# Kernel optimization log

Hardware: AMD Instinct MI355X
Metric: run time of the kernel (lower is better)

The kernel has to match this reference:

```python
import jax, jax.numpy as jnp
import numpy as np

D = 1024
H = 16
HD = D // H
MLP = 4 * D
EPS = 1e-5


def layer_norm(x, g, b):
    mu = jnp.mean(x, axis=-1, keepdims=True)
    var = jnp.mean((x - mu) ** 2, axis=-1, keepdims=True)
    return (x - mu) * jax.lax.rsqrt(var + EPS) * g + b


def grn(stacked, W, b, g, be):
    # stacked: [B, L, S, D]; input-dependent weights + normalized branch, summed over L
    w = jax.nn.relu(jnp.einsum('blsd,de->blse', stacked, W) + b)
    n = layer_norm(stacked, g, be)
    return jnp.sum(w + n, axis=1)  # [B, S, D]


def setup_inputs() -> dict:
    key = jax.random.key(0)
    ks = jax.random.split(key, 24)
    s = 0.02
    inp = {
        'x': jax.random.normal(ks[0], (2, 2048, D), jnp.float32),
        'layer_outputs': jax.random.normal(ks[1], (2, 4, 2048, D), jnp.float32),
    }
    i = 2
    for name in ('q', 'k', 'v'):
        inp[f'grn_{name}_W'] = jax.random.normal(ks[i], (D, D), jnp.float32) * s; i += 1
        inp[f'grn_{name}_b'] = jnp.zeros((D,), jnp.float32)
        inp[f'grn_{name}_g'] = jnp.ones((D,), jnp.float32)
        inp[f'grn_{name}_be'] = jnp.zeros((D,), jnp.float32)
    inp['attn_out_W'] = jax.random.normal(ks[i], (D, D), jnp.float32) * s; i += 1
    inp['attn_out_b'] = jnp.zeros((D,), jnp.float32)
    inp['attn_norm_g'] = jnp.ones((D,), jnp.float32)
    inp['attn_norm_b'] = jnp.zeros((D,), jnp.float32)
    inp['ffn_W1'] = jax.random.normal(ks[i], (D, MLP), jnp.float32) * s; i += 1
    inp['ffn_b1'] = jnp.zeros((MLP,), jnp.float32)
    inp['ffn_W2'] = jax.random.normal(ks[i], (MLP, D), jnp.float32) * s; i += 1
    inp['ffn_b2'] = jnp.zeros((D,), jnp.float32)
    inp['ffn_norm_g'] = jnp.ones((D,), jnp.float32)
    inp['ffn_norm_b'] = jnp.zeros((D,), jnp.float32)
    return inp


def reference(x, layer_outputs,
              grn_q_W, grn_q_b, grn_q_g, grn_q_be,
              grn_k_W, grn_k_b, grn_k_g, grn_k_be,
              grn_v_W, grn_v_b, grn_v_g, grn_v_be,
              attn_out_W, attn_out_b, attn_norm_g, attn_norm_b,
              ffn_W1, ffn_b1, ffn_W2, ffn_b2, ffn_norm_g, ffn_norm_b):
    B, S, _ = x.shape
    q = grn(layer_outputs, grn_q_W, grn_q_b, grn_q_g, grn_q_be)
    k = grn(layer_outputs, grn_k_W, grn_k_b, grn_k_g, grn_k_be)
    v = grn(layer_outputs, grn_v_W, grn_v_b, grn_v_g, grn_v_be)
    # [B, H, S, HD]
    q = q.reshape(B, S, H, HD).transpose(0, 2, 1, 3)
    k = k.reshape(B, S, H, HD).transpose(0, 2, 1, 3)
    v = v.reshape(B, S, H, HD).transpose(0, 2, 1, 3)
    scale = HD ** -0.5
    attn = jnp.einsum('bhqd,bhkd->bhqk', q, k) * scale
    attn = jax.nn.softmax(attn, axis=-1)
    out = jnp.einsum('bhqk,bhkd->bhqd', attn, v)
    out = out.transpose(0, 2, 1, 3).reshape(B, S, D)
    out = out @ attn_out_W + attn_out_b
    out = x + layer_norm(out, attn_norm_g, attn_norm_b)
    h = jax.nn.gelu(out @ ffn_W1 + ffn_b1, approximate=False) @ ffn_W2 + ffn_b2
    out = out + layer_norm(h, ffn_norm_g, ffn_norm_b)
    return out
```

## Files before the change

### kernel.cpp

```cpp
#include <hip/hip_runtime.h>
#include <cstddef>

#define B_  2
#define S_  2048
#define D_  1024
#define L_  4
#define H_  16
#define HD_ 64
#define MLP_ 4096
#define EPS_ 1e-5f

typedef __attribute__((ext_vector_type(8))) short  bf16x8;
typedef __attribute__((ext_vector_type(4))) float  f32x4;

__device__ __forceinline__ unsigned short f2bf(float x) {
    unsigned int u = __float_as_uint(x);
    u = (u + 0x7fffu + ((u >> 16) & 1u)) >> 16;
    return (unsigned short)u;
}
__device__ __forceinline__ float bf2f(unsigned short h) {
    return __uint_as_float(((unsigned int)h) << 16);
}

__global__ __launch_bounds__(256) void wconv_kernel(
    const float* __restrict__ W, unsigned short* __restrict__ Thi,
    unsigned short* __restrict__ Tlo, int K, int N)
{
    __shared__ float T[32][33];
    const int n0 = blockIdx.x * 32, k0 = blockIdx.y * 32;
    const int t = threadIdx.x;
    {
        const int r = t >> 3, c4 = (t & 7) * 4;
        const float4 w = *(const float4*)(W + (size_t)(k0 + r) * N + n0 + c4);
        T[r][c4 + 0] = w.x; T[r][c4 + 1] = w.y;
        T[r][c4 + 2] = w.z; T[r][c4 + 3] = w.w;
    }
    __syncthreads();
    {
        const int n = t >> 3, k4 = (t & 7) * 4;
        ushort4 h, l;
        float f;
        f = T[k4 + 0][n]; h.x = f2bf(f); l.x = f2bf(f - bf2f(h.x));
        f = T[k4 + 1][n]; h.y = f2bf(f); l.y = f2bf(f - bf2f(h.y));
        f = T[k4 + 2][n]; h.z = f2bf(f); l.z = f2bf(f - bf2f(h.z));
        f = T[k4 + 3][n]; h.w = f2bf(f); l.w = f2bf(f - bf2f(h.w));
        *(ushort4*)(Thi + (size_t)(n0 + n) * K + k0 + k4) = h;
        *(ushort4*)(Tlo + (size_t)(n0 + n) * K + k0 + k4) = l;
    }
}

template <int EPI>
__global__ __launch_bounds__(256) void gemm_bf16s_kernel(
    const float* __restrict__ A,
    const unsigned short* __restrict__ Bth, const unsigned short* __restrict__ Btl,
    const float* __restrict__ bias, float* __restrict__ C,
    int M, int N, int K)
{
    __shared__ unsigned short As_hi[128 * 40];
    __shared__ unsigned short As_lo[128 * 40];
    __shared__ unsigned short Bs_hi[128 * 40];
    __shared__ unsigned short Bs_lo[128 * 40];

    const int tid  = threadIdx.x;
    const int lane = tid & 63;
    const int wid  = tid >> 6;
    const int wr   = wid >> 1, wc = wid & 1;
    const int l15  = lane & 15, chunk = lane >> 4;
    const int row0 = blockIdx.y * 128;
    const int col0 = blockIdx.x * 128;

    const int a_off = (wr * 64 + l15) * 40 + chunk * 8;
    const int b_off = (wc * 64 + l15) * 40 + chunk * 8;

    f32x4 acc[4][4] = {};

    for (int k0 = 0; k0 < K; k0 += 32) {
        __syncthreads();
        #pragma unroll
        for (int u = 0; u < 4; ++u) {
            const int idx = tid + u * 256;
            const int r  = idx >> 3;
            const int kc = (idx & 7) * 4;
            const float4 a = *(const float4*)(A + (size_t)(row0 + r) * K + k0 + kc);
            ushort4 h, l;
            h.x = f2bf(a.x); l.x = f2bf(a.x - bf2f(h.x));
            h.y = f2bf(a.y); l.y = f2bf(a.y - bf2f(h.y));
            h.z = f2bf(a.z); l.z = f2bf(a.z - bf2f(h.z));
            h.w = f2bf(a.w); l.w = f2bf(a.w - bf2f(h.w));
            *(ushort4*)&As_hi[r * 40 + kc] = h;
            *(ushort4*)&As_lo[r * 40 + kc] = l;
        }
        #pragma unroll
        for (int u = 0; u < 2; ++u) {
            const int idx = tid + u * 256;
            const int c  = idx >> 2;
            const int kc = (idx & 3) * 8;
            const size_t gb = (size_t)(col0 + c) * K + k0 + kc;
            *(uint4*)&Bs_hi[c * 40 + kc] = *(const uint4*)(Bth + gb);
            *(uint4*)&Bs_lo[c * 40 + kc] = *(const uint4*)(Btl + gb);
        }
        __syncthreads();

        bf16x8 ah[4], al[4], bh[4], bl[4];
        #pragma unroll
        for (int mi = 0; mi < 4; ++mi) {
            ah[mi] = *(const bf16x8*)&As_hi[a_off + mi * 640];
            al[mi] = *(const bf16x8*)&As_lo[a_off + mi * 640];
        }
        #pragma unroll
        for (int ni = 0; ni < 4; ++ni) {
            bh[ni] = *(const bf16x8*)&Bs_hi[b_off + ni * 640];
            bl[ni] = *(const bf16x8*)&Bs_lo[b_off + ni * 640];
        }
        #pragma unroll
        for (int mi = 0; mi < 4; ++mi)
            #pragma unroll
            for (int ni = 0; ni < 4; ++ni) {
                acc[mi][ni] = __builtin_amdgcn_mfma_f32_16x16x32_bf16(
                    ah[mi], bh[ni], acc[mi][ni], 0, 0, 0);
                acc[mi][ni] = __builtin_amdgcn_mfma_f32_16x16x32_bf16(
                    ah[mi], bl[ni], acc[mi][ni], 0, 0, 0);
                acc[mi][ni] = __builtin_amdgcn_mfma_f32_16x16x32_bf16(
                    al[mi], bh[ni], acc[mi][ni], 0, 0, 0);
            }
    }

    const int rbase = row0 + wr * 64 + (lane >> 4) * 4;
    const int cbase = col0 + wc * 64 + l15;
    #pragma unroll
    for (int mi = 0; mi < 4; ++mi) {
        #pragma unroll
        for (int reg = 0; reg < 4; ++reg) {
            const int gr = rbase + mi * 16 + reg;
            #pragma unroll
            for (int ni = 0; ni < 4; ++ni) {
                const int gc = cbase + ni * 16;
                float v = acc[mi][ni][reg] + bias[gc];
                if (EPI == 1) v = fmaxf(v, 0.f);
                else if (EPI == 2) v = 0.5f * v * (1.f + erff(v * 0.70710678118654752f));
                C[(size_t)gr * N + gc] = v;
            }
        }
    }
}

__global__ __launch_bounds__(256) void grn_ns_kernel(
    const float* __restrict__ LO, float* __restrict__ NS)
{
    const int row = blockIdx.x;
    const int b = row >> 11, s = row & (S_ - 1);
    const int tid = threadIdx.x;
    __shared__ float r1[4], r2[4];

    float acc[4] = {0.f, 0.f, 0.f, 0.f};
    #pragma unroll
    for (int l = 0; l < L_; ++l) {
        const float* xr = LO + ((size_t)((b * L_ + l) * S_ + s)) * D_;
        const float4 v = *(const float4*)(xr + tid * 4);
        float s1 = v.x + v.y + v.z + v.w;
        float s2 = v.x * v.x + v.y * v.y + v.z * v.z + v.w * v.w;
        #pragma unroll
        for (int off = 32; off >= 1; off >>= 1) {
            s1 += __shfl_xor(s1, off);
            s2 += __shfl_xor(s2, off);
        }
        if ((tid & 63) == 0) { r1[tid >> 6] = s1; r2[tid >> 6] = s2; }
        __syncthreads();
        s1 = r1[0] + r1[1] + r1[2] + r1[3];
        s2 = r2[0] + r2[1] + r2[2] + r2[3];
        __syncthreads();
        const float mu  = s1 * (1.f / D_);
        const float var = s2 * (1.f / D_) - mu * mu;
        const float rs  = rsqrtf(var + EPS_);
        acc[0] += (v.x - mu) * rs;
        acc[1] += (v.y - mu) * rs;
        acc[2] += (v.z - mu) * rs;
        acc[3] += (v.w - mu) * rs;
    }
    float4 o = {acc[0], acc[1], acc[2], acc[3]};
    *(float4*)(NS + (size_t)row * D_ + tid * 4) = o;
}

__global__ __launch_bounds__(256) void grn_reduce_kernel(
    const float* __restrict__ P, const float* __restrict__ NS,
    const float* __restrict__ g, const float* __restrict__ be,
    float* __restrict__ out)
{
    const size_t i4 = (size_t)blockIdx.x * 256 + threadIdx.x;
    const int d4 = (int)(i4 & (D_ / 4 - 1));
    const size_t row = i4 >> 8;
    const int b = (int)(row >> 11), s = (int)(row & (S_ - 1));

    float4 a = {0.f, 0.f, 0.f, 0.f};
    #pragma unroll
    for (int l = 0; l < L_; ++l) {
        const float4 w = *(const float4*)(P + ((size_t)((b * L_ + l) * S_ + s)) * D_ + d4 * 4);
        a.x += w.x; a.y += w.y; a.z += w.z; a.w += w.w;
    }
    const float4 n  = *(const float4*)(NS + row * D_ + d4 * 4);
    const float4 gg = *(const float4*)(g + d4 * 4);
    const float4 bb = *(const float4*)(be + d4 * 4);
    float4 o;
    o.x = a.x + n.x * gg.x + 4.f * bb.x;
    o.y = a.y + n.y * gg.y + 4.f * bb.y;
    o.z = a.z + n.z * gg.z + 4.f * bb.z;
    o.w = a.w + n.w * gg.w + 4.f * bb.w;
    *(float4*)(out + row * D_ + d4 * 4) = o;
}

__global__ __launch_bounds__(256) void kvconv_kernel(
    const float* __restrict__ Kin, const float* __restrict__ Vin,
    unsigned short* __restrict__ Kh, unsigned short* __restrict__ Kl,
    unsigned short* __restrict__ Vth, unsigned short* __restrict__ Vtl)
{
    __shared__ float T[64][68];
    const int t = threadIdx.x;
    const int st = blockIdx.x;
    const int bh = blockIdx.y;
    const int b = bh >> 4, h = bh & 15;
    const int s0 = st * 64;

    #pragma unroll
    for (int u = 0; u < 4; ++u) {
        const int idx = t + u * 256;
        const int r  = idx >> 4;
        const int c4 = (idx & 15) * 4;
        const size_t src = ((size_t)(b * S_ + s0 + r)) * D_ + h * 64 + c4;
        const float4 kf = *(const float4*)(Kin + src);
        ushort4 hh, ll;
        hh.x = f2bf(kf.x); ll.x = f2bf(kf.x - bf2f(hh.x));
        hh.y = f2bf(kf.y); ll.y = f2bf(kf.y - bf2f(hh.y));
        hh.z = f2bf(kf.z); ll.z = f2bf(kf.z - bf2f(hh.z));
        hh.w = f2bf(kf.w); ll.w = f2bf(kf.w - bf2f(hh.w));
        const size_t kd = ((size_t)bh * S_ + s0 + r) * 64 + c4;
        *(ushort4*)(Kh + kd) = hh;
        *(ushort4*)(Kl + kd) = ll;
        const float4 vf = *(const float4*)(Vin + src);
        T[r][c4 + 0] = vf.x; T[r][c4 + 1] = vf.y;
        T[r][c4 + 2] = vf.z; T[r][c4 + 3] = vf.w;
    }
    __syncthreads();
    #pragma unroll
    for (int u = 0; u < 4; ++u) {
        const int idx = t + u * 256;
        const int d  = idx >> 4;
        const int s4 = (idx & 15) * 4;
        ushort4 hh, ll;
        float f;
        f = T[s4 + 0][d]; hh.x = f2bf(f); ll.x = f2bf(f - bf2f(hh.x));
        f = T[s4 + 1][d]; hh.y = f2bf(f); ll.y = f2bf(f - bf2f(hh.y));
        f = T[s4 + 2][d]; hh.z = f2bf(f); ll.z = f2bf(f - bf2f(hh.z));
        f = T[s4 + 3][d]; hh.w = f2bf(f); ll.w = f2bf(f - bf2f(hh.w));
        const size_t vd = ((size_t)bh * 64 + d) * S_ + s0 + s4;
        *(ushort4*)(Vth + vd) = hh;
        *(ushort4*)(Vtl + vd) = ll;
    }
}

__global__ __launch_bounds__(256) void attn_mfma_kernel(
    const float* __restrict__ Q,
    const unsigned short* __restrict__ Kh, const unsigned short* __restrict__ Kl,
    const unsigned short* __restrict__ Vth, const unsigned short* __restrict__ Vtl,
    float* __restrict__ O)
{
    __shared__ unsigned short Ksh[64 * 72], Ksl[64 * 72];
    __shared__ unsigned short Vsh[64 * 72], Vsl[64 * 72];
    __shared__ unsigned short Phs[4][32 * 72];
    __shared__ unsigned short Pls[4][32 * 72];

    const int tid  = threadIdx.x;
    const int lane = tid & 63;
    const int w    = tid >> 6;
    const int l15  = lane & 15, g = lane >> 4;
    const int bh   = blockIdx.y;
    const int b    = bh >> 4, h = bh & 15;
    const int q0   = blockIdx.x * 128 + w * 32;
    const float scale = 0.125f;

    bf16x8 qh[2][2], ql[2][2];
    #pragma unroll
    for (int mi = 0; mi < 2; ++mi)
        #pragma unroll
        for (int ks = 0; ks < 2; ++ks) {
            const float* qp = Q + ((size_t)(b * S_ + q0 + mi * 16 + l15)) * D_
                              + h * 64 + ks * 32 + g * 8;
            const float4 f0 = *(const float4*)qp;
            const float4 f1 = *(const float4*)(qp + 4);
            const float vs[8] = {f0.x * scale, f0.y * scale, f0.z * scale, f0.w * scale,
                                 f1.x * scale, f1.y * scale, f1.z * scale, f1.w * scale};
            #pragma unroll
            for (int j = 0; j < 8; ++j) {
                const unsigned short hv = f2bf(vs[j]);
                qh[mi][ks][j] = (short)hv;
                ql[mi][ks][j] = (short)f2bf(vs[j] - bf2f(hv));
            }
        }

    f32x4 o[2][4] = {};
    float mrun[2][4], lrun[2][4];
    #pragma unroll
    for (int mi = 0; mi < 2; ++mi)
        #pragma unroll
        for (int r = 0; r < 4; ++r) { mrun[mi][r] = -1e30f; lrun[mi][r] = 0.f; }

    const unsigned short* KhB = Kh  + (size_t)bh * S_ * 64;
    const unsigned short* KlB = Kl  + (size_t)bh * S_ * 64;
    const unsigned short* VhB = Vth + (size_t)bh * 64 * S_;
    const unsigned short* VlB = Vtl + (size_t)bh * 64 * S_;

    for (int kt = 0; kt < S_; kt += 64) {
        __syncthreads();
        #pragma unroll
        for (int u = 0; u < 2; ++u) {
            const int idx = tid + u * 256;
            const int rr  = idx >> 3;
            const int c8  = (idx & 7) * 8;
            *(uint4*)&Ksh[rr * 72 + c8] = *(const uint4*)(KhB + (size_t)(kt + rr) * 64 + c8);
            *(uint4*)&Ksl[rr * 72 + c8] = *(const uint4*)(KlB + (size_t)(kt + rr) * 64 + c8);
            *(uint4*)&Vsh[rr * 72 + c8] = *(const uint4*)(VhB + (size_t)rr * S_ + kt + c8);
            *(uint4*)&Vsl[rr * 72 + c8] = *(const uint4*)(VlB + (size_t)rr * S_ + kt + c8);
        }
        __syncthreads();

        f32x4 s[2][4] = {};
        #pragma unroll
        for (int ks = 0; ks < 2; ++ks)
            #pragma unroll
            for (int ni = 0; ni < 4; ++ni) {
                const bf16x8 khf = *(const bf16x8*)&Ksh[(ni * 16 + l15) * 72 + ks * 32 + g * 8];
                const bf16x8 klf = *(const bf16x8*)&Ksl[(ni * 16 + l15) * 72 + ks * 32 + g * 8];
                #pragma unroll
                for (int mi = 0; mi < 2; ++mi) {
                    s[mi][ni] = __builtin_amdgcn_mfma_f32_16x16x32_bf16(qh[mi][ks], khf, s[mi][ni], 0, 0, 0);
                    s[mi][ni] = __builtin_amdgcn_mfma_f32_16x16x32_bf16(qh[mi][ks], klf, s[mi][ni], 0, 0, 0);
                    s[mi][ni] = __builtin_amdgcn_mfma_f32_16x16x32_bf16(ql[mi][ks], khf, s[mi][ni], 0, 0, 0);
                }
            }

        #pragma unroll
        for (int mi = 0; mi < 2; ++mi) {
            #pragma unroll
            for (int r = 0; r < 4; ++r) {
                float mx = fmaxf(fmaxf(s[mi][0][r], s[mi][1][r]),
                                 fmaxf(s[mi][2][r], s[mi][3][r]));
                mx = fmaxf(mx, __shfl_xor(mx, 1));
                mx = fmaxf(mx, __shfl_xor(mx, 2));
                mx = fmaxf(mx, __shfl_xor(mx, 4));
                mx = fmaxf(mx, __shfl_xor(mx, 8));
                const float mn = fmaxf(mrun[mi][r], mx);
                const float c  = __expf(mrun[mi][r] - mn);
                mrun[mi][r] = mn;
                float rs = 0.f;
                #pragma unroll
                for (int ni = 0; ni < 4; ++ni) {
                    const float p = __expf(s[mi][ni][r] - mn);
                    rs += p;
                    const unsigned short ph = f2bf(p);
                    const int off = (mi * 16 + 4 * g + r) * 72 + ni * 16 + l15;
                    Phs[w][off] = ph;
                    Pls[w][off] = f2bf(p - bf2f(ph));
                }
                rs += __shfl_xor(rs, 1);
                rs += __shfl_xor(rs, 2);
                rs += __shfl_xor(rs, 4);
                rs += __shfl_xor(rs, 8);
                lrun[mi][r] = lrun[mi][r] * c + rs;
                #pragma unroll
                for (int di = 0; di < 4; ++di) o[mi][di][r] *= c;
            }
        }

        #pragma unroll
        for (int ks = 0; ks < 2; ++ks) {
            bf16x8 pfh[2], pfl[2];
            #pragma unroll
            for (int mi = 0; mi < 2; ++mi) {
                pfh[mi] = *(const bf16x8*)&Phs[w][(mi * 16 + l15) * 72 + ks * 32 + g * 8];
                pfl[mi] = *(const bf16x8*)&Pls[w][(mi * 16 + l15) * 72 + ks * 32 + g * 8];
            }
            #pragma unroll
            for (int di = 0; di < 4; ++di) {
                const bf16x8 vhf = *(const bf16x8*)&Vsh[(di * 16 + l15) * 72 + ks * 32 + g * 8];
                const bf16x8 vlf = *(const bf16x8*)&Vsl[(di * 16 + l15) * 72 + ks * 32 + g * 8];
                #pragma unroll
                for (int mi = 0; mi < 2; ++mi) {
                    o[mi][di] = __builtin_amdgcn_mfma_f32_16x16x32_bf16(pfh[mi], vhf, o[mi][di], 0, 0, 0);
                    o[mi][di] = __builtin_amdgcn_mfma_f32_16x16x32_bf16(pfh[mi], vlf, o[mi][di], 0, 0, 0);
                    o[mi][di] = __builtin_amdgcn_mfma_f32_16x16x32_bf16(pfl[mi], vhf, o[mi][di], 0, 0, 0);
                }
            }
        }
    }

    #pragma unroll
    for (int mi = 0; mi < 2; ++mi)
        #pragma unroll
        for (int r = 0; r < 4; ++r) {
            const float inv = 1.f / lrun[mi][r];
            float* op = O + ((size_t)(b * S_ + q0 + mi * 16 + 4 * g + r)) * D_
                        + h * 64 + l15;
            #pragma unroll
            for (int di = 0; di < 4; ++di) op[di * 16] = o[mi][di][r] * inv;
        }
}

__global__ __launch_bounds__(256) void add_ln_kernel(
    const float* __restrict__ Y, const float* __restrict__ R,
    const float* __restrict__ g, const float* __restrict__ beta,
    float* __restrict__ out)
{
    const int row = blockIdx.x;
    const int tid = threadIdx.x;
    __shared__ float r1[4], r2[4];

    const float4 v = *(const float4*)(Y + (size_t)row * D_ + tid * 4);
    float s1 = v.x + v.y + v.z + v.w;
    float s2 = v.x * v.x + v.y * v.y + v.z * v.z + v.w * v.w;
    #pragma unroll
    for (int off = 32; off >= 1; off >>= 1) {
        s1 += __shfl_xor(s1, off);
        s2 += __shfl_xor(s2, off);
    }
    if ((tid & 63) == 0) { r1[tid >> 6] = s1; r2[tid >> 6] = s2; }
    __syncthreads();
    s1 = r1[0] + r1[1] + r1[2] + r1[3];
    s2 = r2[0] + r2[1] + r2[2] + r2[3];
    const float mu  = s1 * (1.f / D_);
    const float var = s2 * (1.f / D_) - mu * mu;
    const float rs  = rsqrtf(var + EPS_);

    const float4 rr = *(const float4*)(R + (size_t)row * D_ + tid * 4);
    const float4 gg = *(const float4*)(g + tid * 4);
    const float4 bb = *(const float4*)(beta + tid * 4);
    float4 o;
    o.x = rr.x + (v.x - mu) * rs * gg.x + bb.x;
    o.y = rr.y + (v.y - mu) * rs * gg.y + bb.y;
    o.z = rr.z + (v.z - mu) * rs * gg.z + bb.z;
    o.w = rr.w + (v.w - mu) * rs * gg.w + bb.w;
    *(float4*)(out + (size_t)row * D_ + tid * 4) = o;
}

extern "C" void kernel_launch(void* const* d_in, const int* in_sizes, int n_in,
                              void* d_out, int out_size, void* d_ws, size_t ws_size,
                              hipStream_t stream)
{
    const float* x  = (const float*)d_in[0];
    const float* LO = (const float*)d_in[1];
    const float* Wq  = (const float*)d_in[2];
    const float* bq_ = (const float*)d_in[3];
    const float* gq  = (const float*)d_in[4];
    const float* beq = (const float*)d_in[5];
    const float* Wk  = (const float*)d_in[6];
    const float* bk_ = (const float*)d_in[7];
    const float* gk  = (const float*)d_in[8];
    const float* bek = (const float*)d_in[9];
    const float* Wv  = (const float*)d_in[10];
    const float* bv_ = (const float*)d_in[11];
    const float* gv  = (const float*)d_in[12];
    const float* bev = (const float*)d_in[13];
    const float* Wo  = (const float*)d_in[14];
    const float* bo  = (const float*)d_in[15];
    const float* ang = (const float*)d_in[16];
    const float* anb = (const float*)d_in[17];
    const float* W1  = (const float*)d_in[18];
    const float* b1  = (const float*)d_in[19];
    const float* W2  = (const float*)d_in[20];
    const float* b2  = (const float*)d_in[21];
    const float* fng = (const float*)d_in[22];
    const float* fnb = (const float*)d_in[23];

    const size_t BS  = (size_t)B_ * S_;
    const size_t SEG = BS * D_;
    float* ws  = (float*)d_ws;
    float* ns   = ws;
    float* bufq = ws + SEG;
    float* bufk = ws + 2 * SEG;
    float* bufv = ws + 3 * SEG;
    float* big  = ws + 4 * SEG;

    unsigned short* wt = (unsigned short*)(ws + 8 * SEG);
    const size_t MM = 1048576;
    unsigned short* wtq_h = wt;            unsigned short* wtq_l = wt + MM;
    unsigned short* wtk_h = wt + 2 * MM;   unsigned short* wtk_l = wt + 3 * MM;
    unsigned short* wtv_h = wt + 4 * MM;   unsigned short* wtv_l = wt + 5 * MM;
    unsigned short* wto_h = wt + 6 * MM;   unsigned short* wto_l = wt + 7 * MM;
    unsigned short* w1_h  = wt + 8 * MM;   unsigned short* w1_l  = wt + 12 * MM;
    unsigned short* w2_h  = wt + 16 * MM;  unsigned short* w2_l  = wt + 20 * MM;

    const size_t KVSEG = (size_t)B_ * H_ * S_ * HD_;
    unsigned short* kv  = (unsigned short*)big;
    unsigned short* kh_ = kv;
    unsigned short* kl_ = kv + KVSEG;
    unsigned short* vth = kv + 2 * KVSEG;
    unsigned short* vtl = kv + 3 * KVSEG;

    const dim3 blk(256);

    wconv_kernel<<<dim3(32, 32),  blk, 0, stream>>>(Wq, wtq_h, wtq_l, D_, D_);
    wconv_kernel<<<dim3(32, 32),  blk, 0, stream>>>(Wk, wtk_h, wtk_l, D_, D_);
    wconv_kernel<<<dim3(32, 32),  blk, 0, stream>>>(Wv, wtv_h, wtv_l, D_, D_);
    wconv_kernel<<<dim3(32, 32),  blk, 0, stream>>>(Wo, wto_h, wto_l, D_, D_);
    wconv_kernel<<<dim3(128, 32), blk, 0, stream>>>(W1, w1_h,  w1_l,  D_, MLP_);
    wconv_kernel<<<dim3(32, 128), blk, 0, stream>>>(W2, w2_h,  w2_l,  MLP_, D_);

    grn_ns_kernel<<<dim3(BS), blk, 0, stream>>>(LO, ns);

    const unsigned short* Wh[3] = {wtq_h, wtk_h, wtv_h};
    const unsigned short* Wl[3] = {wtq_l, wtk_l, wtv_l};
    const float* bp[3]  = {bq_, bk_, bv_};
    const float* gp[3]  = {gq, gk, gv};
    const float* bep[3] = {beq, bek, bev};
    float* outp[3] = {bufq, bufk, bufv};
    for (int p = 0; p < 3; ++p) {
        gemm_bf16s_kernel<1><<<dim3(D_ / 128, (B_ * L_ * S_) / 128), blk, 0, stream>>>(
            LO, Wh[p], Wl[p], bp[p], big, B_ * L_ * S_, D_, D_);
        grn_reduce_kernel<<<dim3(BS), blk, 0, stream>>>(big, ns, gp[p], bep[p], outp[p]);
    }

    kvconv_kernel<<<dim3(S_ / 64, B_ * H_), blk, 0, stream>>>(bufk, bufv, kh_, kl_, vth, vtl);
    attn_mfma_kernel<<<dim3(S_ / 128, B_ * H_), blk, 0, stream>>>(bufq, kh_, kl_, vth, vtl, ns);

    gemm_bf16s_kernel<0><<<dim3(D_ / 128, BS / 128), blk, 0, stream>>>(
        ns, wto_h, wto_l, bo, bufq, (int)BS, D_, D_);

    add_ln_kernel<<<dim3(BS), blk, 0, stream>>>(bufq, x, ang, anb, bufk);

    gemm_bf16s_kernel<2><<<dim3(MLP_ / 128, BS / 128), blk, 0, stream>>>(
        bufk, w1_h, w1_l, b1, big, (int)BS, MLP_, D_);

    gemm_bf16s_kernel<0><<<dim3(D_ / 128, BS / 128), blk, 0, stream>>>(
        big, w2_h, w2_l, b2, bufv, (int)BS, D_, MLP_);

    add_ln_kernel<<<dim3(BS), blk, 0, stream>>>(bufv, bufk, fng, fnb, (float*)d_out);
}
```

Measured before the change: 1.223 ms.

## Pre-split GEMM activations to bf16 pairs, prefetch tiles, swizzle blocks, drop P low part

Activations are converted once to hi/lo bf16 pairs in a separate pass, or written that way by the FFN1 epilogue, so GEMMs load packed bf16 instead of converting fp32 per tile. The GEMM gains register prefetch of the next K tile, an XCD-aware block-index swizzle, and s_setprio around MFMA bursts. Attention drops the low-precision half of P, which removes one MFMA per PV step and its LDS buffer at some accuracy cost. The extra conversion passes add memory traffic and workspace use.

```diff
diff --git a/kernel.cpp b/kernel.cpp
--- a/kernel.cpp
+++ b/kernel.cpp
@@ -20,6 +20,21 @@
 }
 __device__ __forceinline__ float bf2f(unsigned short h) {
     return __uint_as_float(((unsigned int)h) << 16);
+}
+
+__global__ __launch_bounds__(256) void aconv_kernel(
+    const float* __restrict__ X, unsigned short* __restrict__ Xh,
+    unsigned short* __restrict__ Xl)
+{
+    const size_t i4 = (size_t)blockIdx.x * 256 + threadIdx.x;
+    const float4 v = *(const float4*)(X + i4 * 4);
+    ushort4 h, l;
+    h.x = f2bf(v.x); l.x = f2bf(v.x - bf2f(h.x));
+    h.y = f2bf(v.y); l.y = f2bf(v.y - bf2f(h.y));
+    h.z = f2bf(v.z); l.z = f2bf(v.z - bf2f(h.z));
+    h.w = f2bf(v.w); l.w = f2bf(v.w - bf2f(h.w));
+    *(ushort4*)(Xh + i4 * 4) = h;
+    *(ushort4*)(Xl + i4 * 4) = l;
 }
 
 __global__ __launch_bounds__(256) void wconv_kernel(
@@ -49,11 +64,12 @@
     }
 }
 
-template <int EPI>
-__global__ __launch_bounds__(256) void gemm_bf16s_kernel(
-    const float* __restrict__ A,
+template <int EPI, int OUT>
+__global__ __launch_bounds__(256) void gemm_bf16p_kernel(
+    const unsigned short* __restrict__ Ah, const unsigned short* __restrict__ Al,
     const unsigned short* __restrict__ Bth, const unsigned short* __restrict__ Btl,
     const float* __restrict__ bias, float* __restrict__ C,
+    unsigned short* __restrict__ Chi, unsigned short* __restrict__ Clo,
     int M, int N, int K)
 {
     __shared__ unsigned short As_hi[128 * 40];
@@ -66,40 +82,54 @@
     const int wid  = tid >> 6;
     const int wr   = wid >> 1, wc = wid & 1;
     const int l15  = lane & 15, chunk = lane >> 4;
-    const int row0 = blockIdx.y * 128;
-    const int col0 = blockIdx.x * 128;
+
+    const int NX   = N >> 7;
+    const int nblk = (M >> 7) * NX;
+    int bid = blockIdx.x;
+    if ((nblk & 7) == 0) bid = (bid & 7) * (nblk >> 3) + (bid >> 3);
+    const int row0 = (bid / NX) * 128;
+    const int col0 = (bid % NX) * 128;
 
     const int a_off = (wr * 64 + l15) * 40 + chunk * 8;
     const int b_off = (wc * 64 + l15) * 40 + chunk * 8;
 
+    const int sr  = tid >> 2;
+    const int skc = (tid & 3) * 8;
+
     f32x4 acc[4][4] = {};
+    uint4 ra_h[2], ra_l[2], rb_h[2], rb_l[2];
+
+    #pragma unroll
+    for (int u = 0; u < 2; ++u) {
+        const int r = sr + u * 64;
+        const size_t ga = (size_t)(row0 + r) * K + skc;
+        const size_t gb = (size_t)(col0 + r) * K + skc;
+        ra_h[u] = *(const uint4*)(Ah + ga);  ra_l[u] = *(const uint4*)(Al + ga);
+        rb_h[u] = *(const uint4*)(Bth + gb); rb_l[u] = *(const uint4*)(Btl + gb);
+    }
 
     for (int k0 = 0; k0 < K; k0 += 32) {
         __syncthreads();
         #pragma unroll
-        for (int u = 0; u < 4; ++u) {
-            const int idx = tid + u * 256;
-            const int r  = idx >> 3;
-            const int kc = (idx & 7) * 4;
-            const float4 a = *(const float4*)(A + (size_t)(row0 + r) * K + k0 + kc);
-            ushort4 h, l;
-            h.x = f2bf(a.x); l.x = f2bf(a.x - bf2f(h.x));
-            h.y = f2bf(a.y); l.y = f2bf(a.y - bf2f(h.y));
-            h.z = f2bf(a.z); l.z = f2bf(a.z - bf2f(h.z));
-            h.w = f2bf(a.w); l.w = f2bf(a.w - bf2f(h.w));
-            *(ushort4*)&As_hi[r * 40 + kc] = h;
-            *(ushort4*)&As_lo[r * 40 + kc] = l;
-        }
-        #pragma unroll
         for (int u = 0; u < 2; ++u) {
-            const int idx = tid + u * 256;
-            const int c  = idx >> 2;
-            const int kc = (idx & 3) * 8;
-            const size_t gb = (size_t)(col0 + c) * K + k0 + kc;
-            *(uint4*)&Bs_hi[c * 40 + kc] = *(const uint4*)(Bth + gb);
-            *(uint4*)&Bs_lo[c * 40 + kc] = *(const uint4*)(Btl + gb);
+            const int r = sr + u * 64;
+            *(uint4*)&As_hi[r * 40 + skc] = ra_h[u];
+            *(uint4*)&As_lo[r * 40 + skc] = ra_l[u];
+            *(uint4*)&Bs_hi[r * 40 + skc] = rb_h[u];
+            *(uint4*)&Bs_lo[r * 40 + skc] = rb_l[u];
         }
         __syncthreads();
+
+        if (k0 + 32 < K) {
+            #pragma unroll
+            for (int u = 0; u < 2; ++u) {
+                const int r = sr + u * 64;
+                const size_t ga = (size_t)(row0 + r) * K + k0 + 32 + skc;
+                const size_t gb = (size_t)(col0 + r) * K + k0 + 32 + skc;
+                ra_h[u] = *(const uint4*)(Ah + ga);  ra_l[u] = *(const uint4*)(Al + ga);
+                rb_h[u] = *(const uint4*)(Bth + gb); rb_l[u] = *(const uint4*)(Btl + gb);
+            }
+        }
 
         bf16x8 ah[4], al[4], bh[4], bl[4];
         #pragma unroll
@@ -112,6 +142,7 @@
             bh[ni] = *(const bf16x8*)&Bs_hi[b_off + ni * 640];
             bl[ni] = *(const bf16x8*)&Bs_lo[b_off + ni * 640];
         }
+        __builtin_amdgcn_s_setprio(1);
         #pragma unroll
         for (int mi = 0; mi < 4; ++mi)
             #pragma unroll
@@ -123,6 +154,7 @@
                 acc[mi][ni] = __builtin_amdgcn_mfma_f32_16x16x32_bf16(
                     al[mi], bh[ni], acc[mi][ni], 0, 0, 0);
             }
+        __builtin_amdgcn_s_setprio(0);
     }
 
     const int rbase = row0 + wr * 64 + (lane >> 4) * 4;
@@ -138,7 +170,13 @@
                 float v = acc[mi][ni][reg] + bias[gc];
                 if (EPI == 1) v = fmaxf(v, 0.f);
                 else if (EPI == 2) v = 0.5f * v * (1.f + erff(v * 0.70710678118654752f));
-                C[(size_t)gr * N + gc] = v;
+                if (OUT == 0) {
+                    C[(size_t)gr * N + gc] = v;
+                } else {
+                    const unsigned short hv = f2bf(v);
+                    Chi[(size_t)gr * N + gc] = hv;
+                    Clo[(size_t)gr * N + gc] = f2bf(v - bf2f(hv));
+                }
             }
         }
     }
@@ -266,7 +304,6 @@
     __shared__ unsigned short Ksh[64 * 72], Ksl[64 * 72];
     __shared__ unsigned short Vsh[64 * 72], Vsl[64 * 72];
     __shared__ unsigned short Phs[4][32 * 72];
-    __shared__ unsigned short Pls[4][32 * 72];
 
     const int tid  = threadIdx.x;
     const int lane = tid & 63;
@@ -329,12 +366,14 @@
             for (int ni = 0; ni < 4; ++ni) {
                 const bf16x8 khf = *(const bf16x8*)&Ksh[(ni * 16 + l15) * 72 + ks * 32 + g * 8];
                 const bf16x8 klf = *(const bf16x8*)&Ksl[(ni * 16 + l15) * 72 + ks * 32 + g * 8];
+                __builtin_amdgcn_s_setprio(1);
                 #pragma unroll
                 for (int mi = 0; mi < 2; ++mi) {
                     s[mi][ni] = __builtin_amdgcn_mfma_f32_16x16x32_bf16(qh[mi][ks], khf, s[mi][ni], 0, 0, 0);
                     s[mi][ni] = __builtin_amdgcn_mfma_f32_16x16x32_bf16(qh[mi][ks], klf, s[mi][ni], 0, 0, 0);
                     s[mi][ni] = __builtin_amdgcn_mfma_f32_16x16x32_bf16(ql[mi][ks], khf, s[mi][ni], 0, 0, 0);
                 }
+                __builtin_amdgcn_s_setprio(0);
             }
 
         #pragma unroll
@@ -355,10 +394,7 @@
                 for (int ni = 0; ni < 4; ++ni) {
                     const float p = __expf(s[mi][ni][r] - mn);
                     rs += p;
-                    const unsigned short ph = f2bf(p);
-                    const int off = (mi * 16 + 4 * g + r) * 72 + ni * 16 + l15;
-                    Phs[w][off] = ph;
-                    Pls[w][off] = f2bf(p - bf2f(ph));
+                    Phs[w][(mi * 16 + 4 * g + r) * 72 + ni * 16 + l15] = f2bf(p);
                 }
                 rs += __shfl_xor(rs, 1);
                 rs += __shfl_xor(rs, 2);
@@ -372,22 +408,21 @@
 
         #pragma unroll
         for (int ks = 0; ks < 2; ++ks) {
-            bf16x8 pfh[2], pfl[2];
-            #pragma unroll
-            for (int mi = 0; mi < 2; ++mi) {
+            bf16x8 pfh[2];
+            #pragma unroll
+            for (int mi = 0; mi < 2; ++mi)
                 pfh[mi] = *(const bf16x8*)&Phs[w][(mi * 16 + l15) * 72 + ks * 32 + g * 8];
-                pfl[mi] = *(const bf16x8*)&Pls[w][(mi * 16 + l15) * 72 + ks * 32 + g * 8];
-            }
             #pragma unroll
             for (int di = 0; di < 4; ++di) {
                 const bf16x8 vhf = *(const bf16x8*)&Vsh[(di * 16 + l15) * 72 + ks * 32 + g * 8];
                 const bf16x8 vlf = *(const bf16x8*)&Vsl[(di * 16 + l15) * 72 + ks * 32 + g * 8];
+                __builtin_amdgcn_s_setprio(1);
                 #pragma unroll
                 for (int mi = 0; mi < 2; ++mi) {
                     o[mi][di] = __builtin_amdgcn_mfma_f32_16x16x32_bf16(pfh[mi], vhf, o[mi][di], 0, 0, 0);
                     o[mi][di] = __builtin_amdgcn_mfma_f32_16x16x32_bf16(pfh[mi], vlf, o[mi][di], 0, 0, 0);
-                    o[mi][di] = __builtin_amdgcn_mfma_f32_16x16x32_bf16(pfl[mi], vhf, o[mi][di], 0, 0, 0);
                 }
+                __builtin_amdgcn_s_setprio(0);
             }
         }
     }
@@ -486,6 +521,8 @@
     unsigned short* wto_h = wt + 6 * MM;   unsigned short* wto_l = wt + 7 * MM;
     unsigned short* w1_h  = wt + 8 * MM;   unsigned short* w1_l  = wt + 12 * MM;
     unsigned short* w2_h  = wt + 16 * MM;  unsigned short* w2_l  = wt + 20 * MM;
+    unsigned short* lo_h = wt + 24 * MM;
+    unsigned short* lo_l = lo_h + 16 * MM;
 
     const size_t KVSEG = (size_t)B_ * H_ * S_ * HD_;
     unsigned short* kv  = (unsigned short*)big;
@@ -493,6 +530,12 @@
     unsigned short* kl_ = kv + KVSEG;
     unsigned short* vth = kv + 2 * KVSEG;
     unsigned short* vtl = kv + 3 * KVSEG;
+    unsigned short* hid_h = (unsigned short*)big;
+    unsigned short* hid_l = hid_h + 16 * MM;
+    unsigned short* ns_h = (unsigned short*)bufv;
+    unsigned short* ns_l = ns_h + 4 * MM;
+    unsigned short* r1_h = (unsigned short*)bufq;
+    unsigned short* r1_l = r1_h + 4 * MM;
 
     const dim3 blk(256);
 
@@ -502,6 +545,7 @@
     wconv_kernel<<<dim3(32, 32),  blk, 0, stream>>>(Wo, wto_h, wto_l, D_, D_);
     wconv_kernel<<<dim3(128, 32), blk, 0, stream>>>(W1, w1_h,  w1_l,  D_, MLP_);
     wconv_kernel<<<dim3(32, 128), blk, 0, stream>>>(W2, w2_h,  w2_l,  MLP_, D_);
+    aconv_kernel<<<dim3(16384), blk, 0, stream>>>(LO, lo_h, lo_l);
 
     grn_ns_kernel<<<dim3(BS), blk, 0, stream>>>(LO, ns);
 
@@ -511,25 +555,29 @@
     const float* gp[3]  = {gq, gk, gv};
     const float* bep[3] = {beq, bek, bev};
     float* outp[3] = {bufq, bufk, bufv};
+    const int grnBlocks = (D_ / 128) * ((B_ * L_ * S_) / 128);
     for (int p = 0; p < 3; ++p) {
-        gemm_bf16s_kernel<1><<<dim3(D_ / 128, (B_ * L_ * S_) / 128), blk, 0, stream>>>(
-            LO, Wh[p], Wl[p], bp[p], big, B_ * L_ * S_, D_, D_);
+        gemm_bf16p_kernel<1, 0><<<dim3(grnBlocks), blk, 0, stream>>>(
+            lo_h, lo_l, Wh[p], Wl[p], bp[p], big, nullptr, nullptr,
+            B_ * L_ * S_, D_, D_);
         grn_reduce_kernel<<<dim3(BS), blk, 0, stream>>>(big, ns, gp[p], bep[p], outp[p]);
     }
 
     kvconv_kernel<<<dim3(S_ / 64, B_ * H_), blk, 0, stream>>>(bufk, bufv, kh_, kl_, vth, vtl);
     attn_mfma_kernel<<<dim3(S_ / 128, B_ * H_), blk, 0, stream>>>(bufq, kh_, kl_, vth, vtl, ns);
 
-    gemm_bf16s_kernel<0><<<dim3(D_ / 128, BS / 128), blk, 0, stream>>>(
-        ns, wto_h, wto_l, bo, bufq, (int)BS, D_, D_);
+    aconv_kernel<<<dim3(4096), blk, 0, stream>>>(ns, ns_h, ns_l);
+    gemm_bf16p_kernel<0, 0><<<dim3((D_ / 128) * (BS / 128)), blk, 0, stream>>>(
+        ns_h, ns_l, wto_h, wto_l, bo, bufq, nullptr, nullptr, (int)BS, D_, D_);
 
     add_ln_kernel<<<dim3(BS), blk, 0, stream>>>(bufq, x, ang, anb, bufk);
 
-    gemm_bf16s_kernel<2><<<dim3(MLP_ / 128, BS / 128), blk, 0, stream>>>(
-        bufk, w1_h, w1_l, b1, big, (int)BS, MLP_, D_);
-
-    gemm_bf16s_kernel<0><<<dim3(D_ / 128, BS / 128), blk, 0, stream>>>(
-        big, w2_h, w2_l, b2, bufv, (int)BS, D_, MLP_);
+    aconv_kernel<<<dim3(4096), blk, 0, stream>>>(bufk, r1_h, r1_l);
+    gemm_bf16p_kernel<2, 1><<<dim3((MLP_ / 128) * (BS / 128)), blk, 0, stream>>>(
+        r1_h, r1_l, w1_h, w1_l, b1, nullptr, hid_h, hid_l, (int)BS, MLP_, D_);
+
+    gemm_bf16p_kernel<0, 0><<<dim3((D_ / 128) * (BS / 128)), blk, 0, stream>>>(
+        hid_h, hid_l, w2_h, w2_l, b2, bufv, nullptr, nullptr, (int)BS, D_, MLP_);
 
     add_ln_kernel<<<dim3(BS), blk, 0, stream>>>(bufv, bufk, fng, fnb, (float*)d_out);
 }
```

After: 2.592 ms. 2.12x slower.
